# Kernel optimization log

Hardware: AMD Instinct MI355X
Metric: run time of the kernel (lower is better)

## Reference

```python
import math
import jax, jax.numpy as jnp
import numpy as np

N_HEADS = 8

def setup_inputs() -> dict:
    key = jax.random.key(0)
    qkv = jax.random.normal(key, (4, 3 * N_HEADS * 64, 2048), dtype=jnp.float32)
    return {"qkv": qkv}

def reference(qkv) -> jnp.ndarray:
    bs, width, length = qkv.shape
    assert width % (3 * N_HEADS) == 0
    ch = width // (3 * N_HEADS)
    q, k, v = jnp.split(qkv, 3, axis=1)            # each [N, H*C, T]
    scale = 1.0 / math.sqrt(math.sqrt(ch))
    qh = (q * scale).reshape(bs * N_HEADS, ch, length)  # [BH, C, T]
    kh = (k * scale).reshape(bs * N_HEADS, ch, length)
    vh = v.reshape(bs * N_HEADS, ch, length)
    weight = jnp.einsum('bct,bcs->bts', qh, kh)    # [BH, T, T]
    weight = jax.nn.softmax(weight.astype(jnp.float32), axis=-1).astype(weight.dtype)
    a = jnp.einsum('bts,bcs->bct', weight, vh)     # [BH, C, T]
    return a.reshape(bs, -1, length)
```

## Files before the change

### kernel.cpp

```cpp
#include <hip/hip_runtime.h>

#define T_LEN 2048
#define CH 64
#define NH 8
#define STILE 64
#define TTILE 128
#define WT 32
#define NIT (T_LEN / STILE)
#define CSK 68
#define CS 72
#define QS 132
#define RS 68

#define QSCALE 0.180336880972948929f

typedef __attribute__((ext_vector_type(4))) float  f32x4;
typedef __attribute__((ext_vector_type(8))) __bf16 bf16x8;
typedef __attribute__((ext_vector_type(4))) __bf16 bf16x4;
typedef __attribute__((ext_vector_type(2))) __bf16 bf16x2;
typedef __attribute__((ext_vector_type(2))) unsigned int uint2v;
typedef __attribute__((ext_vector_type(4))) unsigned int uint4v;

union SMem {
  float qstage[CH * QS];
  struct {
    __bf16 k_hi[2][STILE * CSK];
    __bf16 v_s [2][CH * CS];
  } loop;
  struct {
    float o[4][WT][RS];
    float l[4][2][4][16];
  } red;
};

#define MFMA(A, B, C) __builtin_amdgcn_mfma_f32_16x16x32_bf16((A), (B), (C), 0, 0, 0)

__device__ __forceinline__ unsigned pkbf2(float lo, float hi) {
  bf16x2 t = {(__bf16)lo, (__bf16)hi};
  return __builtin_bit_cast(unsigned, t);
}

__device__ __forceinline__ void load_k(const float* kp, int s0, int tid, float2 (&kreg)[4]) {
  int cq  = tid >> 5;
  int sp2 = tid & 31;
  const float* kc = kp + (size_t)(4 * cq) * T_LEN + s0 + 2 * sp2;
#pragma unroll
  for (int r = 0; r < 4; ++r)
    kreg[r] = *(const float2*)(kc + (size_t)r * T_LEN);
}

__device__ __forceinline__ void store_k(__bf16* kh, int tid, const float2 (&kreg)[4]) {
  int cq  = tid >> 5;
  int sp2 = tid & 31;
  bf16x4 w0 = {(__bf16)kreg[0].x, (__bf16)kreg[1].x, (__bf16)kreg[2].x, (__bf16)kreg[3].x};
  bf16x4 w1 = {(__bf16)kreg[0].y, (__bf16)kreg[1].y, (__bf16)kreg[2].y, (__bf16)kreg[3].y};
  *(bf16x4*)&kh[(2 * sp2 + 0) * CSK + 4 * cq] = w0;
  *(bf16x4*)&kh[(2 * sp2 + 1) * CSK + 4 * cq] = w1;
}

__device__ __forceinline__ void load_v(const float* vp, int s0, int tid, f32x4 (&vreg)[2]) {
#pragma unroll
  for (int rr = 0; rr < 2; ++rr) {
    int fidx = rr * 512 + tid;
    int c  = fidx >> 4;
    int s4 = (fidx & 15) << 2;
    vreg[rr] = *(const f32x4*)(vp + (size_t)c * T_LEN + s0 + s4);
  }
}

__device__ __forceinline__ void store_v(__bf16* vs, int tid, const f32x4 (&vreg)[2]) {
#pragma unroll
  for (int rr = 0; rr < 2; ++rr) {
    int fidx = rr * 512 + tid;
    int c  = fidx >> 4;
    int s4 = (fidx & 15) << 2;
    bf16x4 vv = {(__bf16)vreg[rr].x, (__bf16)vreg[rr].y,
                 (__bf16)vreg[rr].z, (__bf16)vreg[rr].w};
    *(bf16x4*)&vs[c * CS + s4] = vv;
  }
}

__global__ __launch_bounds__(512, 4)
void qkv_attn_mfma(const float* __restrict__ qkv, float* __restrict__ out) {
  __shared__ SMem sm;
  const int tid  = threadIdx.x;
  const int lane = tid & 63;
  const int wave = tid >> 6;
  const int wt   = wave & 3;
  const int ws   = wave >> 2;
  const int tn   = lane & 15;
  const int quad = lane >> 4;

  const int d0 = blockIdx.x;
  const int w  = ((d0 & 7) << 6) | (d0 >> 3);
  const int ttile = w & 15;
  const int bh    = w >> 4;
  const int b = bh >> 3, h = bh & 7;
  const size_t base = (size_t)b * (3 * NH * CH) * T_LEN;
  const float* qp = qkv + base + (size_t)(CH * h) * T_LEN;
  const float* kp = qkv + base + (size_t)(CH * (NH + h)) * T_LEN;
  const float* vp = qkv + base + (size_t)(CH * (2 * NH + h)) * T_LEN;
  const int t0 = ttile * TTILE;

#pragma unroll
  for (int rr = 0; rr < 4; ++rr) {
    int fidx = rr * 512 + tid;
    int c  = fidx >> 5;
    int t4 = (fidx & 31) << 2;
    f32x4 q4 = *(const f32x4*)(qp + (size_t)c * T_LEN + t0 + t4);
    *(f32x4*)&sm.qstage[c * QS + t4] = q4;
  }
  __syncthreads();

  bf16x8 qh[2][2];
#pragma unroll
  for (int nb = 0; nb < 2; ++nb)
#pragma unroll
    for (int kb = 0; kb < 2; ++kb) {
      int tloc = wt * WT + nb * 16 + tn;
      bf16x8 H;
#pragma unroll
      for (int j = 0; j < 8; ++j) {
        float qv = sm.qstage[(kb * 32 + quad * 8 + j) * QS + tloc] * QSCALE;
        H[j] = (__bf16)qv;
      }
      qh[nb][kb] = H;
    }
  __syncthreads();

  f32x4 acc[4][2];
  float l_part[2] = {0.f, 0.f};
#pragma unroll
  for (int mbc = 0; mbc < 4; ++mbc)
#pragma unroll
    for (int nb = 0; nb < 2; ++nb)
      acc[mbc][nb] = (f32x4){0.f, 0.f, 0.f, 0.f};

  float2 kreg[4];
  f32x4  vreg[2];
  load_k(kp, 0, tid, kreg);
  load_v(vp, 0, tid, vreg);
  store_k(sm.loop.k_hi[0], tid, kreg);
  store_v(sm.loop.v_s[0], tid, vreg);
  __syncthreads();

  for (int it = 0; it < NIT; ++it) {
    const int cur = it & 1;
    const bool more = (it + 1 < NIT);

    if (more) {
      load_k(kp, (it + 1) * STILE, tid, kreg);
      load_v(vp, (it + 1) * STILE, tid, vreg);
    }

    const __bf16* kh = sm.loop.k_hi[cur];
    bf16x8 ah[2][2];
#pragma unroll
    for (int mb = 0; mb < 2; ++mb) {
      const int srow = (32 * ws + 16 * mb + tn) * CSK;
#pragma unroll
      for (int kb = 0; kb < 2; ++kb) {
        bf16x4 a0 = *(const bf16x4*)&kh[srow + 32 * kb + quad * 8];
        bf16x4 a1 = *(const bf16x4*)&kh[srow + 32 * kb + quad * 8 + 4];
        ah[mb][kb] = __builtin_shufflevector(a0, a1, 0, 1, 2, 3, 4, 5, 6, 7);
      }
    }
    f32x4 d[2][2];
#pragma unroll
    for (int mb = 0; mb < 2; ++mb)
#pragma unroll
      for (int nb = 0; nb < 2; ++nb) {
        f32x4 t = (f32x4){0.f, 0.f, 0.f, 0.f};
        t = MFMA(ah[mb][0], qh[nb][0], t);
        t = MFMA(ah[mb][1], qh[nb][1], t);
        d[mb][nb] = t;
      }

    const __bf16* vs = sm.loop.v_s[cur];
    bf16x8 av[4];
#pragma unroll
    for (int mbc = 0; mbc < 4; ++mbc)
      av[mbc] = *(const bf16x8*)&vs[(16 * mbc + tn) * CS + 32 * ws + quad * 8];

    bf16x8 bp[2];
#pragma unroll
    for (int nb = 0; nb < 2; ++nb) {
      float rs = 0.f;
#pragma unroll
      for (int mb = 0; mb < 2; ++mb)
#pragma unroll
        for (int r = 0; r < 4; ++r) {
          float e = __builtin_amdgcn_exp2f(d[mb][nb][r]);
          d[mb][nb][r] = e;
          rs += e;
        }
      l_part[nb] += rs;
      unsigned u00 = pkbf2(d[0][nb][0], d[0][nb][1]);
      unsigned u01 = pkbf2(d[0][nb][2], d[0][nb][3]);
      unsigned u10 = pkbf2(d[1][nb][0], d[1][nb][1]);
      unsigned u11 = pkbf2(d[1][nb][2], d[1][nb][3]);
      uint2v s0 = __builtin_amdgcn_permlane32_swap(u00, u10, false, false);
      uint2v r0 = __builtin_amdgcn_permlane16_swap(s0.x, s0.y, false, false);
      uint2v s1 = __builtin_amdgcn_permlane32_swap(u01, u11, false, false);
      uint2v r1 = __builtin_amdgcn_permlane16_swap(s1.x, s1.y, false, false);
      uint4v wv = {r0.x, r1.x, r0.y, r1.y};
      bp[nb] = __builtin_bit_cast(bf16x8, wv);
    }

#pragma unroll
    for (int mbc = 0; mbc < 4; ++mbc)
#pragma unroll
      for (int nb = 0; nb < 2; ++nb)
        acc[mbc][nb] = MFMA(av[mbc], bp[nb], acc[mbc][nb]);

    if (more) {
      store_k(sm.loop.k_hi[cur ^ 1], tid, kreg);
      store_v(sm.loop.v_s [cur ^ 1], tid, vreg);
    }
    __syncthreads();
  }

  if (ws == 1) {
#pragma unroll
    for (int nb = 0; nb < 2; ++nb) {
      sm.red.l[wt][nb][quad][tn] = l_part[nb];
#pragma unroll
      for (int mbc = 0; mbc < 4; ++mbc)
        *(f32x4*)&sm.red.o[wt][nb * 16 + tn][16 * mbc + quad * 4] = acc[mbc][nb];
    }
  }
  __syncthreads();
  if (ws == 0) {
    float* op = out + (size_t)bh * CH * T_LEN;
#pragma unroll
    for (int nb = 0; nb < 2; ++nb) {
      float l = l_part[nb] + sm.red.l[wt][nb][quad][tn];
      l += __shfl_xor(l, 16, 64);
      l += __shfl_xor(l, 32, 64);
      float inv_l = 1.0f / l;
      int t = t0 + wt * WT + nb * 16 + tn;
#pragma unroll
      for (int mbc = 0; mbc < 4; ++mbc) {
        f32x4 o = acc[mbc][nb] + *(const f32x4*)&sm.red.o[wt][nb * 16 + tn][16 * mbc + quad * 4];
        o = o * inv_l;
        int c = 16 * mbc + quad * 4;
        op[(size_t)(c + 0) * T_LEN + t] = o.x;
        op[(size_t)(c + 1) * T_LEN + t] = o.y;
        op[(size_t)(c + 2) * T_LEN + t] = o.z;
        op[(size_t)(c + 3) * T_LEN + t] = o.w;
      }
    }
  }
}

extern "C" void kernel_launch(void* const* d_in, const int* in_sizes, int n_in,
                              void* d_out, int out_size, void* d_ws, size_t ws_size,
                              hipStream_t stream) {
  const float* qkv = (const float*)d_in[0];
  float* out = (float*)d_out;
  dim3 grid(512);
  qkv_attn_mfma<<<grid, 512, 0, stream>>>(qkv, out);
}
```

Before: 123.5 us.

## Double query tile per block to 256 and split K/V loading across wave groups

```diff
diff --git a/kernel.cpp b/kernel.cpp
--- a/kernel.cpp
+++ b/kernel.cpp
@@ -4,12 +4,12 @@
 #define CH 64
 #define NH 8
 #define STILE 64
-#define TTILE 128
+#define TTILE 256
 #define WT 32
 #define NIT (T_LEN / STILE)
 #define CSK 68
 #define CS 72
-#define QS 132
+#define QS 260
 #define RS 68
 
 #define QSCALE 0.180336880972948929f
@@ -28,8 +28,8 @@
     __bf16 v_s [2][CH * CS];
   } loop;
   struct {
-    float o[4][WT][RS];
-    float l[4][2][4][16];
+    float o[8][WT][RS];
+    float l[2][8][4][16];
   } red;
 };
 
@@ -40,38 +40,38 @@
   return __builtin_bit_cast(unsigned, t);
 }
 
-__device__ __forceinline__ void load_k(const float* kp, int s0, int tid, float2 (&kreg)[4]) {
-  int cq  = tid >> 5;
-  int sp2 = tid & 31;
+__device__ __forceinline__ void load_k(const float* kp, int s0, int ltid, float2 (&kreg)[4]) {
+  int cq  = ltid >> 5;
+  int sp2 = ltid & 31;
   const float* kc = kp + (size_t)(4 * cq) * T_LEN + s0 + 2 * sp2;
 #pragma unroll
   for (int r = 0; r < 4; ++r)
     kreg[r] = *(const float2*)(kc + (size_t)r * T_LEN);
 }
 
-__device__ __forceinline__ void store_k(__bf16* kh, int tid, const float2 (&kreg)[4]) {
-  int cq  = tid >> 5;
-  int sp2 = tid & 31;
+__device__ __forceinline__ void store_k(__bf16* kh, int ltid, const float2 (&kreg)[4]) {
+  int cq  = ltid >> 5;
+  int sp2 = ltid & 31;
   bf16x4 w0 = {(__bf16)kreg[0].x, (__bf16)kreg[1].x, (__bf16)kreg[2].x, (__bf16)kreg[3].x};
   bf16x4 w1 = {(__bf16)kreg[0].y, (__bf16)kreg[1].y, (__bf16)kreg[2].y, (__bf16)kreg[3].y};
   *(bf16x4*)&kh[(2 * sp2 + 0) * CSK + 4 * cq] = w0;
   *(bf16x4*)&kh[(2 * sp2 + 1) * CSK + 4 * cq] = w1;
 }
 
-__device__ __forceinline__ void load_v(const float* vp, int s0, int tid, f32x4 (&vreg)[2]) {
+__device__ __forceinline__ void load_v(const float* vp, int s0, int ltid, f32x4 (&vreg)[2]) {
 #pragma unroll
   for (int rr = 0; rr < 2; ++rr) {
-    int fidx = rr * 512 + tid;
+    int fidx = rr * 512 + ltid;
     int c  = fidx >> 4;
     int s4 = (fidx & 15) << 2;
     vreg[rr] = *(const f32x4*)(vp + (size_t)c * T_LEN + s0 + s4);
   }
 }
 
-__device__ __forceinline__ void store_v(__bf16* vs, int tid, const f32x4 (&vreg)[2]) {
+__device__ __forceinline__ void store_v(__bf16* vs, int ltid, const f32x4 (&vreg)[2]) {
 #pragma unroll
   for (int rr = 0; rr < 2; ++rr) {
-    int fidx = rr * 512 + tid;
+    int fidx = rr * 512 + ltid;
     int c  = fidx >> 4;
     int s4 = (fidx & 15) << 2;
     bf16x4 vv = {(__bf16)vreg[rr].x, (__bf16)vreg[rr].y,
@@ -80,21 +80,22 @@
   }
 }
 
-__global__ __launch_bounds__(512, 4)
+__global__ __launch_bounds__(1024, 4)
 void qkv_attn_mfma(const float* __restrict__ qkv, float* __restrict__ out) {
   __shared__ SMem sm;
   const int tid  = threadIdx.x;
   const int lane = tid & 63;
   const int wave = tid >> 6;
-  const int wt   = wave & 3;
-  const int ws   = wave >> 2;
+  const int wt   = wave & 7;
+  const int ws   = wave >> 3;
   const int tn   = lane & 15;
   const int quad = lane >> 4;
+  const int stid = tid & 511;
 
   const int d0 = blockIdx.x;
-  const int w  = ((d0 & 7) << 6) | (d0 >> 3);
-  const int ttile = w & 15;
-  const int bh    = w >> 4;
+  const int w  = ((d0 & 7) << 5) | (d0 >> 3);
+  const int ttile = w & 7;
+  const int bh    = w >> 3;
   const int b = bh >> 3, h = bh & 7;
   const size_t base = (size_t)b * (3 * NH * CH) * T_LEN;
   const float* qp = qkv + base + (size_t)(CH * h) * T_LEN;
@@ -104,9 +105,9 @@
 
 #pragma unroll
   for (int rr = 0; rr < 4; ++rr) {
-    int fidx = rr * 512 + tid;
-    int c  = fidx >> 5;
-    int t4 = (fidx & 31) << 2;
+    int fidx = rr * 1024 + tid;
+    int c  = fidx >> 6;
+    int t4 = (fidx & 63) << 2;
     f32x4 q4 = *(const f32x4*)(qp + (size_t)c * T_LEN + t0 + t4);
     *(f32x4*)&sm.qstage[c * QS + t4] = q4;
   }
@@ -138,10 +139,8 @@
 
   float2 kreg[4];
   f32x4  vreg[2];
-  load_k(kp, 0, tid, kreg);
-  load_v(vp, 0, tid, vreg);
-  store_k(sm.loop.k_hi[0], tid, kreg);
-  store_v(sm.loop.v_s[0], tid, vreg);
+  if (ws == 0) { load_k(kp, 0, stid, kreg); store_k(sm.loop.k_hi[0], stid, kreg); }
+  else         { load_v(vp, 0, stid, vreg); store_v(sm.loop.v_s[0], stid, vreg); }
   __syncthreads();
 
   for (int it = 0; it < NIT; ++it) {
@@ -149,8 +148,8 @@
     const bool more = (it + 1 < NIT);
 
     if (more) {
-      load_k(kp, (it + 1) * STILE, tid, kreg);
-      load_v(vp, (it + 1) * STILE, tid, vreg);
+      if (ws == 0) load_k(kp, (it + 1) * STILE, stid, kreg);
+      else         load_v(vp, (it + 1) * STILE, stid, vreg);
     }
 
     const __bf16* kh = sm.loop.k_hi[cur];
@@ -214,8 +213,8 @@
         acc[mbc][nb] = MFMA(av[mbc], bp[nb], acc[mbc][nb]);
 
     if (more) {
-      store_k(sm.loop.k_hi[cur ^ 1], tid, kreg);
-      store_v(sm.loop.v_s [cur ^ 1], tid, vreg);
+      if (ws == 0) store_k(sm.loop.k_hi[cur ^ 1], stid, kreg);
+      else         store_v(sm.loop.v_s [cur ^ 1], stid, vreg);
     }
     __syncthreads();
   }
@@ -223,7 +222,7 @@
   if (ws == 1) {
 #pragma unroll
     for (int nb = 0; nb < 2; ++nb) {
-      sm.red.l[wt][nb][quad][tn] = l_part[nb];
+      sm.red.l[nb][wt][quad][tn] = l_part[nb];
 #pragma unroll
       for (int mbc = 0; mbc < 4; ++mbc)
         *(f32x4*)&sm.red.o[wt][nb * 16 + tn][16 * mbc + quad * 4] = acc[mbc][nb];
@@ -234,7 +233,7 @@
     float* op = out + (size_t)bh * CH * T_LEN;
 #pragma unroll
     for (int nb = 0; nb < 2; ++nb) {
-      float l = l_part[nb] + sm.red.l[wt][nb][quad][tn];
+      float l = l_part[nb] + sm.red.l[nb][wt][quad][tn];
       l += __shfl_xor(l, 16, 64);
       l += __shfl_xor(l, 32, 64);
       float inv_l = 1.0f / l;
@@ -258,6 +257,6 @@
                               hipStream_t stream) {
   const float* qkv = (const float*)d_in[0];
   float* out = (float*)d_out;
-  dim3 grid(512);
-  qkv_attn_mfma<<<grid, 512, 0, stream>>>(qkv, out);
-}
+  dim3 grid(256);
+  qkv_attn_mfma<<<grid, 1024, 0, stream>>>(qkv, out);
+}
```

Measured after the change: 120.0 us. 1.03x faster.
